# Kernel tuning notes

Hardware: AMD Instinct MI355X
Metric: run time of the kernel (lower is better)

## Reference

```python
import jax, jax.numpy as jnp
import numpy as np

N, IN_F, H, F = 4096, 256, 8, 64
NEG_INF = -1e9  # stand-in for -inf; avoids NaNs for fully-masked rows


def setup_inputs() -> dict:
    key = jax.random.key(0)
    k1, k2, k3, k4, k5 = jax.random.split(key, 5)
    h = jax.random.normal(k1, (N, IN_F), dtype=jnp.float32)
    adj = jax.random.randint(k2, (N, N), 0, 2, dtype=jnp.int32)
    # xavier-ish scaled params
    W = jax.random.normal(k3, (IN_F, H * F), dtype=jnp.float32) * (2.0 / (IN_F + H * F)) ** 0.5
    a_src = jax.random.normal(k4, (H, F), dtype=jnp.float32) * (2.0 / (H * F)) ** 0.5
    a_dst = jax.random.normal(k5, (H, F), dtype=jnp.float32) * (2.0 / (H * F)) ** 0.5
    bias = jnp.zeros((H * F,), dtype=jnp.float32)
    return {"h": h, "adj": adj, "W": W, "a_src": a_src, "a_dst": a_dst, "bias": bias}


def reference(h, adj, W, a_src, a_dst, bias):
    # Wh: [N, H, F]
    Wh = (h @ W).reshape(N, H, F)
    e_src = jnp.einsum('nhf,hf->nh', Wh, a_src)  # [N, H]
    e_dst = jnp.einsum('nhf,hf->nh', Wh, a_dst)  # [N, H]
    e = e_src[:, None, :] + e_dst[None, :, :]    # [N, N, H]
    e = jnp.where(e > 0, e, 0.2 * e)             # LeakyReLU(0.2)
    e = jnp.where((adj != 0)[:, :, None], e, NEG_INF)
    alpha = jax.nn.softmax(e, axis=1)            # softmax over neighbors j
    # h_prime[i,h,f] = sum_j alpha[i,j,h] * Wh[j,h,f]
    h_prime = jnp.einsum('ijh,jhf->ihf', alpha, Wh)
    h_prime = h_prime.reshape(N, H * F)          # concat=True
    return h_prime + bias
```

## Files before the change

kernel.cpp:

```cpp
#include <hip/hip_runtime.h>
#include <stdint.h>

#define NN   4096
#define KIN  256
#define NH   8
#define FD   64
#define HFD  512
#define NC   2
#define BI   32
#define JT   64
#define NT   ((NN / NC) / JT)

typedef __attribute__((ext_vector_type(4))) float  floatx4;
typedef __attribute__((ext_vector_type(8))) short  short8;

__device__ __forceinline__ unsigned short f2bf_rne(float x) {
    uint32_t u = __float_as_uint(x);
    u += 0x7FFFu + ((u >> 16) & 1u);
    return (unsigned short)(u >> 16);
}

__device__ __forceinline__ uint32_t packtrunc(float lo, float hi) {
    return (__float_as_uint(hi) & 0xFFFF0000u) | (__float_as_uint(lo) >> 16);
}

__global__ __launch_bounds__(256) void k1_front(
        const float* __restrict__ hmat, const float* __restrict__ Wmat,
        const float* __restrict__ a_src, const float* __restrict__ a_dst,
        unsigned short* __restrict__ whbT,
        float* __restrict__ esrcT, float* __restrict__ edstT) {
    __shared__ float As[64][36];
    __shared__ float Bs[32][64];
    __shared__ float scrS[64][16];
    __shared__ float scrD[64][16];
    const int tid = threadIdx.x;
    const int n0  = blockIdx.x * 64;
    const int hd  = blockIdx.y;
    const int hf0 = hd * 64;
    const int r0  = (tid >> 4) * 4;
    const int c0  = (tid & 15) * 4;
    float acc[4][4] = {};
    for (int k0 = 0; k0 < KIN; k0 += 32) {
        #pragma unroll
        for (int u = 0; u < 2; ++u) {
            const int v = tid * 2 + u;
            const int r = v >> 3, kk = (v & 7) * 4;
            *reinterpret_cast<float4*>(&As[r][kk]) =
                *reinterpret_cast<const float4*>(&hmat[(size_t)(n0 + r) * KIN + k0 + kk]);
        }
        #pragma unroll
        for (int u = 0; u < 2; ++u) {
            const int v = tid * 2 + u;
            const int kk = v >> 4, cc = (v & 15) * 4;
            *reinterpret_cast<float4*>(&Bs[kk][cc]) =
                *reinterpret_cast<const float4*>(&Wmat[(size_t)(k0 + kk) * HFD + hf0 + cc]);
        }
        __syncthreads();
        #pragma unroll
        for (int k = 0; k < 32; ++k) {
            const float4 b = *reinterpret_cast<const float4*>(&Bs[k][c0]);
            float av[4];
            #pragma unroll
            for (int i = 0; i < 4; ++i) av[i] = As[r0 + i][k];
            #pragma unroll
            for (int i = 0; i < 4; ++i) {
                acc[i][0] += av[i] * b.x;
                acc[i][1] += av[i] * b.y;
                acc[i][2] += av[i] * b.z;
                acc[i][3] += av[i] * b.w;
            }
        }
        __syncthreads();
    }
    #pragma unroll
    for (int j = 0; j < 4; ++j) {
        const int f = c0 + j;
        ushort4 w4;
        w4.x = f2bf_rne(acc[0][j]); w4.y = f2bf_rne(acc[1][j]);
        w4.z = f2bf_rne(acc[2][j]); w4.w = f2bf_rne(acc[3][j]);
        *reinterpret_cast<ushort4*>(&whbT[(size_t)(hf0 + f) * NN + n0 + r0]) = w4;
    }
    float as4[4], ad4[4];
    #pragma unroll
    for (int j = 0; j < 4; ++j) { as4[j] = a_src[hf0 + c0 + j]; ad4[j] = a_dst[hf0 + c0 + j]; }
    #pragma unroll
    for (int i = 0; i < 4; ++i) {
        float ps = 0.f, pd = 0.f;
        #pragma unroll
        for (int j = 0; j < 4; ++j) { ps += acc[i][j] * as4[j]; pd += acc[i][j] * ad4[j]; }
        scrS[r0 + i][tid & 15] = ps;
        scrD[r0 + i][tid & 15] = pd;
    }
    __syncthreads();
    if (tid < 64) {
        float s = 0.f, d = 0.f;
        #pragma unroll
        for (int q = 0; q < 16; ++q) { s += scrS[tid][q]; d += scrD[tid][q]; }
        esrcT[hd * NN + n0 + tid] = s;
        edstT[hd * NN + n0 + tid] = d;
    }
}

__global__ __launch_bounds__(256) void k2_tables(
        const float* __restrict__ esrcT, const float* __restrict__ edstT,
        float* __restrict__ es1T, float* __restrict__ es2T,
        float* __restrict__ ed1T, float* __restrict__ ed2T) {
    __shared__ float red[256];
    const int hd = blockIdx.x, tid = threadIdx.x;
    float m = -1e30f;
    for (int n = tid; n < NN; n += 256) m = fmaxf(m, edstT[hd * NN + n]);
    red[tid] = m;
    __syncthreads();
    for (int s = 128; s > 0; s >>= 1) {
        if (tid < s) red[tid] = fmaxf(red[tid], red[tid + s]);
        __syncthreads();
    }
    const float maxd = red[0];
    for (int n = tid; n < NN; n += 256) {
        const float ed = edstT[hd * NN + n];
        ed1T[hd * NN + n] = __expf(ed);
        ed2T[hd * NN + n] = __expf(0.2f * ed);
        const float es = esrcT[hd * NN + n];
        const float t  = es + maxd;
        const float M  = fmaxf(t, 0.2f * t);
        es1T[hd * NN + n] = __expf(es - M);
        es2T[hd * NN + n] = __expf(0.2f * es - M);
    }
}

__global__ __launch_bounds__(512) void k3_attn(
        const int* __restrict__ adj, const unsigned short* __restrict__ whbT,
        const float* __restrict__ es1T, const float* __restrict__ es2T,
        const float* __restrict__ ed1T, const float* __restrict__ ed2T,
        float* __restrict__ numP, float* __restrict__ denP) {
    __shared__ uint32_t amask[BI][32];
    const int tid  = threadIdx.x;
    const int lane = tid & 63;
    const int wid  = tid >> 6;
    const int iblk = blockIdx.x & 127;
    const int jc   = blockIdx.x >> 7;
    const int i0   = iblk * BI;
    const int jbase = jc * (NN / NC);
    const int g  = lane >> 4;
    const int lr = lane & 15;

    float es1[2], es2[2];
    #pragma unroll
    for (int mi = 0; mi < 2; ++mi) {
        es1[mi] = es1T[wid * NN + i0 + mi * 16 + lr];
        es2[mi] = es2T[wid * NN + i0 + mi * 16 + lr];
    }

    floatx4 acc[2][4] = {};
    floatx4 accd[2] = {};

    short8 ones;
    {
        const short ov = (lr == 0) ? (short)0x3F80 : (short)0;
        #pragma unroll
        for (int e = 0; e < 8; ++e) ones[e] = ov;
    }

    for (int t = 0; t < NT; ++t) {
        const int j0 = jbase + t * JT;
        __syncthreads();
        {
            const int r = tid >> 4, q = tid & 15;
            const int4 a = *reinterpret_cast<const int4*>(&adj[(size_t)(i0 + r) * NN + j0 + q * 4]);
            const uint32_t m0 = (a.x ? 0xFFFFu : 0u) | (a.y ? 0xFFFF0000u : 0u);
            const uint32_t m1 = (a.z ? 0xFFFFu : 0u) | (a.w ? 0xFFFF0000u : 0u);
            const int w0 = q * 2;
            const int p0 = (w0 & 3) | ((((w0 >> 2) ^ (r & 7)) & 7) << 2);
            amask[r][p0]     = m0;
            amask[r][p0 + 1] = m1;
        }
        __syncthreads();

        short8 bfrag[2][4];
        #pragma unroll
        for (int ks = 0; ks < 2; ++ks)
            #pragma unroll
            for (int ni = 0; ni < 4; ++ni)
                bfrag[ks][ni] = *reinterpret_cast<const short8*>(
                    &whbT[(size_t)(wid * FD + ni * 16 + lr) * NN + j0 + ks * 32 + g * 8]);

        #pragma unroll
        for (int ks = 0; ks < 2; ++ks) {
            const int jo = wid * NN + j0 + ks * 32 + g * 8;
            const float4 e1a = *reinterpret_cast<const float4*>(&ed1T[jo]);
            const float4 e1b = *reinterpret_cast<const float4*>(&ed1T[jo + 4]);
            const float4 e2a = *reinterpret_cast<const float4*>(&ed2T[jo]);
            const float4 e2b = *reinterpret_cast<const float4*>(&ed2T[jo + 4]);
            #pragma unroll
            for (int mi = 0; mi < 2; ++mi) {
                const int rr = mi * 16 + lr;
                const int pb = (((ks * 4 + g) ^ (lr & 7)) & 7) * 4;
                const uint4 msk = *reinterpret_cast<const uint4*>(&amask[rr][pb]);
                union { uint32_t w[4]; short8 s8; } pu;
                pu.w[0] = packtrunc(fmaxf(es1[mi] * e1a.x, es2[mi] * e2a.x),
                                    fmaxf(es1[mi] * e1a.y, es2[mi] * e2a.y)) & msk.x;
                pu.w[1] = packtrunc(fmaxf(es1[mi] * e1a.z, es2[mi] * e2a.z),
                                    fmaxf(es1[mi] * e1a.w, es2[mi] * e2a.w)) & msk.y;
                pu.w[2] = packtrunc(fmaxf(es1[mi] * e1b.x, es2[mi] * e2b.x),
                                    fmaxf(es1[mi] * e1b.y, es2[mi] * e2b.y)) & msk.z;
                pu.w[3] = packtrunc(fmaxf(es1[mi] * e1b.z, es2[mi] * e2b.z),
                                    fmaxf(es1[mi] * e1b.w, es2[mi] * e2b.w)) & msk.w;
                #pragma unroll
                for (int ni = 0; ni < 4; ++ni)
                    acc[mi][ni] = __builtin_amdgcn_mfma_f32_16x16x32_bf16(
                        pu.s8, bfrag[ks][ni], acc[mi][ni], 0, 0, 0);
                accd[mi] = __builtin_amdgcn_mfma_f32_16x16x32_bf16(
                        pu.s8, ones, accd[mi], 0, 0, 0);
            }
        }
    }

    #pragma unroll
    for (int mi = 0; mi < 2; ++mi) {
        #pragma unroll
        for (int ni = 0; ni < 4; ++ni) {
            #pragma unroll
            for (int r = 0; r < 4; ++r) {
                const int i = i0 + mi * 16 + g * 4 + r;
                numP[((size_t)jc * NN + i) * HFD + wid * FD + ni * 16 + lr] = acc[mi][ni][r];
            }
        }
        if (lr == 0) {
            #pragma unroll
            for (int r = 0; r < 4; ++r) {
                const int i = i0 + mi * 16 + g * 4 + r;
                denP[((size_t)jc * NH + wid) * NN + i] = accd[mi][r];
            }
        }
    }
}

__global__ __launch_bounds__(256) void k4_reduce(
        const float* __restrict__ numP, const float* __restrict__ denP,
        const float* __restrict__ bias, float* __restrict__ out) {
    const int idx = blockIdx.x * 256 + threadIdx.x;
    const int e0 = idx * 4;
    const int i  = e0 >> 9;
    const int hf = e0 & 511;
    const int hd = hf >> 6;
    float4 s = make_float4(0.f, 0.f, 0.f, 0.f);
    float d = 0.f;
    #pragma unroll
    for (int c = 0; c < NC; ++c) {
        const float4 v = *reinterpret_cast<const float4*>(&numP[((size_t)c * NN + i) * HFD + hf]);
        s.x += v.x; s.y += v.y; s.z += v.z; s.w += v.w;
        d += denP[((size_t)c * NH + hd) * NN + i];
    }
    const float inv = 1.0f / d;
    const float4 b = *reinterpret_cast<const float4*>(&bias[hf]);
    float4 o;
    o.x = s.x * inv + b.x; o.y = s.y * inv + b.y;
    o.z = s.z * inv + b.z; o.w = s.w * inv + b.w;
    *reinterpret_cast<float4*>(&out[(size_t)i * HFD + hf]) = o;
}

extern "C" void kernel_launch(void* const* d_in, const int* in_sizes, int n_in,
                              void* d_out, int out_size, void* d_ws, size_t ws_size,
                              hipStream_t stream) {
    const float* hmat  = (const float*)d_in[0];
    const int*   adj   = (const int*)d_in[1];
    const float* Wmat  = (const float*)d_in[2];
    const float* a_src = (const float*)d_in[3];
    const float* a_dst = (const float*)d_in[4];
    const float* bias  = (const float*)d_in[5];
    float* out = (float*)d_out;

    char* ws = (char*)d_ws;
    unsigned short* whbT = (unsigned short*)ws;
    float* esrcT = (float*)(ws + (4u << 20));
    float* edstT = esrcT + NH * NN;
    float* es1T  = edstT + NH * NN;
    float* es2T  = es1T + NH * NN;
    float* ed1T  = es2T + NH * NN;
    float* ed2T  = ed1T + NH * NN;
    float* numP  = ed2T + NH * NN;
    float* denP  = numP + (size_t)NC * NN * HFD;

    k1_front<<<dim3(64, 8), 256, 0, stream>>>(hmat, Wmat, a_src, a_dst, whbT, esrcT, edstT);
    k2_tables<<<dim3(NH), 256, 0, stream>>>(esrcT, edstT, es1T, es2T, ed1T, ed2T);
    k3_attn<<<dim3(128 * NC), 512, 0, stream>>>(adj, whbT, es1T, es2T, ed1T, ed2T, numP, denP);
    k4_reduce<<<dim3((NN * HFD / 4) / 256), 256, 0, stream>>>(numP, denP, bias, out);
}
```

Baseline: 233.7 us.

## Use split-bf16 MFMA projection, smaller attention tiles, double-buffered mask, atomic reduction

```diff
diff --git a/kernel.cpp b/kernel.cpp
--- a/kernel.cpp
+++ b/kernel.cpp
@@ -6,8 +6,8 @@
 #define NH   8
 #define FD   64
 #define HFD  512
-#define NC   2
-#define BI   32
+#define NC   4
+#define BI   16
 #define JT   64
 #define NT   ((NN / NC) / JT)
 
@@ -19,85 +19,107 @@
     u += 0x7FFFu + ((u >> 16) & 1u);
     return (unsigned short)(u >> 16);
 }
-
+__device__ __forceinline__ float bf2f(unsigned short b) {
+    return __uint_as_float(((uint32_t)b) << 16);
+}
 __device__ __forceinline__ uint32_t packtrunc(float lo, float hi) {
     return (__float_as_uint(hi) & 0xFFFF0000u) | (__float_as_uint(lo) >> 16);
 }
 
+__global__ __launch_bounds__(256) void k_zero(float* __restrict__ outAcc,
+                                              float* __restrict__ denA) {
+    const int idx = blockIdx.x * 256 + threadIdx.x;
+    const float4 z = make_float4(0.f, 0.f, 0.f, 0.f);
+    if (idx < (NN * HFD) / 4) {
+        *reinterpret_cast<float4*>(&outAcc[idx * 4]) = z;
+    } else {
+        const int q = idx - (NN * HFD) / 4;
+        if (q < (NH * NN) / 4) *reinterpret_cast<float4*>(&denA[q * 4]) = z;
+    }
+}
+
+__global__ __launch_bounds__(256) void k0_prep(
+        const float* __restrict__ hmat, const float* __restrict__ Wmat,
+        unsigned short* __restrict__ h_hi, unsigned short* __restrict__ h_lo,
+        unsigned short* __restrict__ wt_hi, unsigned short* __restrict__ wt_lo) {
+    const int bx = blockIdx.x, tid = threadIdx.x;
+    if (bx < 1024) {
+        const int e0 = (bx * 256 + tid) * 4;
+        const float4 v = *reinterpret_cast<const float4*>(&hmat[e0]);
+        ushort4 hi, lo;
+        hi.x = f2bf_rne(v.x); lo.x = f2bf_rne(v.x - bf2f(hi.x));
+        hi.y = f2bf_rne(v.y); lo.y = f2bf_rne(v.y - bf2f(hi.y));
+        hi.z = f2bf_rne(v.z); lo.z = f2bf_rne(v.z - bf2f(hi.z));
+        hi.w = f2bf_rne(v.w); lo.w = f2bf_rne(v.w - bf2f(hi.w));
+        *reinterpret_cast<ushort4*>(&h_hi[e0]) = hi;
+        *reinterpret_cast<ushort4*>(&h_lo[e0]) = lo;
+    } else {
+        const int c = bx - 1024;
+        const float v = Wmat[(size_t)tid * HFD + c];
+        const unsigned short hi = f2bf_rne(v);
+        const unsigned short lo = f2bf_rne(v - bf2f(hi));
+        wt_hi[c * KIN + tid] = hi;
+        wt_lo[c * KIN + tid] = lo;
+    }
+}
+
 __global__ __launch_bounds__(256) void k1_front(
-        const float* __restrict__ hmat, const float* __restrict__ Wmat,
+        const unsigned short* __restrict__ h_hi, const unsigned short* __restrict__ h_lo,
+        const unsigned short* __restrict__ wt_hi, const unsigned short* __restrict__ wt_lo,
         const float* __restrict__ a_src, const float* __restrict__ a_dst,
         unsigned short* __restrict__ whbT,
         float* __restrict__ esrcT, float* __restrict__ edstT) {
-    __shared__ float As[64][36];
-    __shared__ float Bs[32][64];
-    __shared__ float scrS[64][16];
-    __shared__ float scrD[64][16];
-    const int tid = threadIdx.x;
+    const int tid  = threadIdx.x;
+    const int w    = tid >> 6;
+    const int lane = tid & 63;
+    const int g = lane >> 4, lr = lane & 15;
     const int n0  = blockIdx.x * 64;
     const int hd  = blockIdx.y;
-    const int hf0 = hd * 64;
-    const int r0  = (tid >> 4) * 4;
-    const int c0  = (tid & 15) * 4;
-    float acc[4][4] = {};
+    const int hf0 = hd * FD;
+    const int row = n0 + w * 16 + lr;
+    floatx4 acc[4] = {};
+    #pragma unroll
     for (int k0 = 0; k0 < KIN; k0 += 32) {
-        #pragma unroll
-        for (int u = 0; u < 2; ++u) {
-            const int v = tid * 2 + u;
-            const int r = v >> 3, kk = (v & 7) * 4;
-            *reinterpret_cast<float4*>(&As[r][kk]) =
-                *reinterpret_cast<const float4*>(&hmat[(size_t)(n0 + r) * KIN + k0 + kk]);
-        }
-        #pragma unroll
-        for (int u = 0; u < 2; ++u) {
-            const int v = tid * 2 + u;
-            const int kk = v >> 4, cc = (v & 15) * 4;
-            *reinterpret_cast<float4*>(&Bs[kk][cc]) =
-                *reinterpret_cast<const float4*>(&Wmat[(size_t)(k0 + kk) * HFD + hf0 + cc]);
-        }
-        __syncthreads();
-        #pragma unroll
-        for (int k = 0; k < 32; ++k) {
-            const float4 b = *reinterpret_cast<const float4*>(&Bs[k][c0]);
-            float av[4];
-            #pragma unroll
-            for (int i = 0; i < 4; ++i) av[i] = As[r0 + i][k];
-            #pragma unroll
-            for (int i = 0; i < 4; ++i) {
-                acc[i][0] += av[i] * b.x;
-                acc[i][1] += av[i] * b.y;
-                acc[i][2] += av[i] * b.z;
-                acc[i][3] += av[i] * b.w;
-            }
-        }
-        __syncthreads();
-    }
-    #pragma unroll
-    for (int j = 0; j < 4; ++j) {
-        const int f = c0 + j;
-        ushort4 w4;
-        w4.x = f2bf_rne(acc[0][j]); w4.y = f2bf_rne(acc[1][j]);
-        w4.z = f2bf_rne(acc[2][j]); w4.w = f2bf_rne(acc[3][j]);
-        *reinterpret_cast<ushort4*>(&whbT[(size_t)(hf0 + f) * NN + n0 + r0]) = w4;
-    }
-    float as4[4], ad4[4];
-    #pragma unroll
-    for (int j = 0; j < 4; ++j) { as4[j] = a_src[hf0 + c0 + j]; ad4[j] = a_dst[hf0 + c0 + j]; }
-    #pragma unroll
-    for (int i = 0; i < 4; ++i) {
+        const short8 ahi = *reinterpret_cast<const short8*>(&h_hi[(size_t)row * KIN + k0 + g * 8]);
+        const short8 alo = *reinterpret_cast<const short8*>(&h_lo[(size_t)row * KIN + k0 + g * 8]);
+        #pragma unroll
+        for (int ni = 0; ni < 4; ++ni) {
+            const size_t bo = (size_t)(hf0 + ni * 16 + lr) * KIN + k0 + g * 8;
+            const short8 bhi = *reinterpret_cast<const short8*>(&wt_hi[bo]);
+            const short8 blo = *reinterpret_cast<const short8*>(&wt_lo[bo]);
+            acc[ni] = __builtin_amdgcn_mfma_f32_16x16x32_bf16(ahi, bhi, acc[ni], 0, 0, 0);
+            acc[ni] = __builtin_amdgcn_mfma_f32_16x16x32_bf16(ahi, blo, acc[ni], 0, 0, 0);
+            acc[ni] = __builtin_amdgcn_mfma_f32_16x16x32_bf16(alo, bhi, acc[ni], 0, 0, 0);
+        }
+    }
+    #pragma unroll
+    for (int ni = 0; ni < 4; ++ni) {
+        const int hf = hf0 + ni * 16 + lr;
+        ushort4 o;
+        o.x = f2bf_rne(acc[ni][0]); o.y = f2bf_rne(acc[ni][1]);
+        o.z = f2bf_rne(acc[ni][2]); o.w = f2bf_rne(acc[ni][3]);
+        *reinterpret_cast<ushort4*>(&whbT[(size_t)hf * NN + n0 + w * 16 + g * 4]) = o;
+    }
+    float asv[4], adv[4];
+    #pragma unroll
+    for (int ni = 0; ni < 4; ++ni) {
+        asv[ni] = a_src[hf0 + ni * 16 + lr];
+        adv[ni] = a_dst[hf0 + ni * 16 + lr];
+    }
+    #pragma unroll
+    for (int r = 0; r < 4; ++r) {
         float ps = 0.f, pd = 0.f;
         #pragma unroll
-        for (int j = 0; j < 4; ++j) { ps += acc[i][j] * as4[j]; pd += acc[i][j] * ad4[j]; }
-        scrS[r0 + i][tid & 15] = ps;
-        scrD[r0 + i][tid & 15] = pd;
-    }
-    __syncthreads();
-    if (tid < 64) {
-        float s = 0.f, d = 0.f;
-        #pragma unroll
-        for (int q = 0; q < 16; ++q) { s += scrS[tid][q]; d += scrD[tid][q]; }
-        esrcT[hd * NN + n0 + tid] = s;
-        edstT[hd * NN + n0 + tid] = d;
+        for (int ni = 0; ni < 4; ++ni) { ps += acc[ni][r] * asv[ni]; pd += acc[ni][r] * adv[ni]; }
+        #pragma unroll
+        for (int off = 1; off < 16; off <<= 1) {
+            ps += __shfl_xor(ps, off, 64);
+            pd += __shfl_xor(pd, off, 64);
+        }
+        if (lr == 0) {
+            esrcT[hd * NN + n0 + w * 16 + g * 4 + r] = ps;
+            edstT[hd * NN + n0 + w * 16 + g * 4 + r] = pd;
+        }
     }
 }
 
@@ -128,32 +150,27 @@
     }
 }
 
-__global__ __launch_bounds__(512) void k3_attn(
+__global__ __launch_bounds__(512, 8) void k3_attn(
         const int* __restrict__ adj, const unsigned short* __restrict__ whbT,
         const float* __restrict__ es1T, const float* __restrict__ es2T,
         const float* __restrict__ ed1T, const float* __restrict__ ed2T,
-        float* __restrict__ numP, float* __restrict__ denP) {
-    __shared__ uint32_t amask[BI][32];
+        float* __restrict__ outAcc, float* __restrict__ denA) {
+    __shared__ uint32_t amask[2][BI][32];
     const int tid  = threadIdx.x;
     const int lane = tid & 63;
     const int wid  = tid >> 6;
-    const int iblk = blockIdx.x & 127;
-    const int jc   = blockIdx.x >> 7;
+    const int iblk = blockIdx.x & 255;
+    const int jc   = blockIdx.x >> 8;
     const int i0   = iblk * BI;
     const int jbase = jc * (NN / NC);
     const int g  = lane >> 4;
     const int lr = lane & 15;
 
-    float es1[2], es2[2];
-    #pragma unroll
-    for (int mi = 0; mi < 2; ++mi) {
-        es1[mi] = es1T[wid * NN + i0 + mi * 16 + lr];
-        es2[mi] = es2T[wid * NN + i0 + mi * 16 + lr];
-    }
-
-    floatx4 acc[2][4] = {};
-    floatx4 accd[2] = {};
-
+    const float es1 = es1T[wid * NN + i0 + lr];
+    const float es2 = es2T[wid * NN + i0 + lr];
+
+    floatx4 acc[4] = {};
+    floatx4 accd = {};
     short8 ones;
     {
         const short ov = (lr == 0) ? (short)0x3F80 : (short)0;
@@ -161,20 +178,22 @@
         for (int e = 0; e < 8; ++e) ones[e] = ov;
     }
 
+    const int sr = tid >> 5, sw = tid & 31;
+    const int spos = (sw & 3) | ((((sw >> 2) ^ (sr & 7)) & 7) << 2);
+    const int* aptr = &adj[(size_t)(i0 + sr) * NN + sw * 2];
+
+    int2 R = *reinterpret_cast<const int2*>(aptr + jbase);
+    amask[0][sr][spos] = (R.x ? 0xFFFFu : 0u) | (R.y ? 0xFFFF0000u : 0u);
+    R = *reinterpret_cast<const int2*>(aptr + jbase + JT);
+    __syncthreads();
+
     for (int t = 0; t < NT; ++t) {
-        const int j0 = jbase + t * JT;
-        __syncthreads();
-        {
-            const int r = tid >> 4, q = tid & 15;
-            const int4 a = *reinterpret_cast<const int4*>(&adj[(size_t)(i0 + r) * NN + j0 + q * 4]);
-            const uint32_t m0 = (a.x ? 0xFFFFu : 0u) | (a.y ? 0xFFFF0000u : 0u);
-            const uint32_t m1 = (a.z ? 0xFFFFu : 0u) | (a.w ? 0xFFFF0000u : 0u);
-            const int w0 = q * 2;
-            const int p0 = (w0 & 3) | ((((w0 >> 2) ^ (r & 7)) & 7) << 2);
-            amask[r][p0]     = m0;
-            amask[r][p0 + 1] = m1;
-        }
-        __syncthreads();
+        const int j0  = jbase + t * JT;
+        const int buf = t & 1;
+        if (t + 1 < NT)
+            amask[(t + 1) & 1][sr][spos] = (R.x ? 0xFFFFu : 0u) | (R.y ? 0xFFFF0000u : 0u);
+        if (t + 2 < NT)
+            R = *reinterpret_cast<const int2*>(aptr + jbase + (t + 2) * JT);
 
         short8 bfrag[2][4];
         #pragma unroll
@@ -191,72 +210,54 @@
             const float4 e1b = *reinterpret_cast<const float4*>(&ed1T[jo + 4]);
             const float4 e2a = *reinterpret_cast<const float4*>(&ed2T[jo]);
             const float4 e2b = *reinterpret_cast<const float4*>(&ed2T[jo + 4]);
+            const int pb = (((ks * 4 + g) ^ (lr & 7)) & 7) * 4;
+            const uint4 msk = *reinterpret_cast<const uint4*>(&amask[buf][lr][pb]);
+            union { uint32_t wd[4]; short8 s8; } pu;
+            pu.wd[0] = packtrunc(fmaxf(es1 * e1a.x, es2 * e2a.x),
+                                 fmaxf(es1 * e1a.y, es2 * e2a.y)) & msk.x;
+            pu.wd[1] = packtrunc(fmaxf(es1 * e1a.z, es2 * e2a.z),
+                                 fmaxf(es1 * e1a.w, es2 * e2a.w)) & msk.y;
+            pu.wd[2] = packtrunc(fmaxf(es1 * e1b.x, es2 * e2b.x),
+                                 fmaxf(es1 * e1b.y, es2 * e2b.y)) & msk.z;
+            pu.wd[3] = packtrunc(fmaxf(es1 * e1b.z, es2 * e2b.z),
+                                 fmaxf(es1 * e1b.w, es2 * e2b.w)) & msk.w;
             #pragma unroll
-            for (int mi = 0; mi < 2; ++mi) {
-                const int rr = mi * 16 + lr;
-                const int pb = (((ks * 4 + g) ^ (lr & 7)) & 7) * 4;
-                const uint4 msk = *reinterpret_cast<const uint4*>(&amask[rr][pb]);
-                union { uint32_t w[4]; short8 s8; } pu;
-                pu.w[0] = packtrunc(fmaxf(es1[mi] * e1a.x, es2[mi] * e2a.x),
-                                    fmaxf(es1[mi] * e1a.y, es2[mi] * e2a.y)) & msk.x;
-                pu.w[1] = packtrunc(fmaxf(es1[mi] * e1a.z, es2[mi] * e2a.z),
-                                    fmaxf(es1[mi] * e1a.w, es2[mi] * e2a.w)) & msk.y;
-                pu.w[2] = packtrunc(fmaxf(es1[mi] * e1b.x, es2[mi] * e2b.x),
-                                    fmaxf(es1[mi] * e1b.y, es2[mi] * e2b.y)) & msk.z;
-                pu.w[3] = packtrunc(fmaxf(es1[mi] * e1b.z, es2[mi] * e2b.z),
-                                    fmaxf(es1[mi] * e1b.w, es2[mi] * e2b.w)) & msk.w;
-                #pragma unroll
-                for (int ni = 0; ni < 4; ++ni)
-                    acc[mi][ni] = __builtin_amdgcn_mfma_f32_16x16x32_bf16(
-                        pu.s8, bfrag[ks][ni], acc[mi][ni], 0, 0, 0);
-                accd[mi] = __builtin_amdgcn_mfma_f32_16x16x32_bf16(
-                        pu.s8, ones, accd[mi], 0, 0, 0);
-            }
-        }
-    }
-
-    #pragma unroll
-    for (int mi = 0; mi < 2; ++mi) {
-        #pragma unroll
-        for (int ni = 0; ni < 4; ++ni) {
-            #pragma unroll
-            for (int r = 0; r < 4; ++r) {
-                const int i = i0 + mi * 16 + g * 4 + r;
-                numP[((size_t)jc * NN + i) * HFD + wid * FD + ni * 16 + lr] = acc[mi][ni][r];
-            }
-        }
-        if (lr == 0) {
-            #pragma unroll
-            for (int r = 0; r < 4; ++r) {
-                const int i = i0 + mi * 16 + g * 4 + r;
-                denP[((size_t)jc * NH + wid) * NN + i] = accd[mi][r];
-            }
-        }
-    }
-}
-
-__global__ __launch_bounds__(256) void k4_reduce(
-        const float* __restrict__ numP, const float* __restrict__ denP,
-        const float* __restrict__ bias, float* __restrict__ out) {
+            for (int ni = 0; ni < 4; ++ni)
+                acc[ni] = __builtin_amdgcn_mfma_f32_16x16x32_bf16(
+                    pu.s8, bfrag[ks][ni], acc[ni], 0, 0, 0);
+            accd = __builtin_amdgcn_mfma_f32_16x16x32_bf16(pu.s8, ones, accd, 0, 0, 0);
+        }
+        __syncthreads();
+    }
+
+    #pragma unroll
+    for (int ni = 0; ni < 4; ++ni)
+        #pragma unroll
+        for (int r = 0; r < 4; ++r)
+            atomicAdd(&outAcc[(size_t)(i0 + g * 4 + r) * HFD + wid * FD + ni * 16 + lr],
+                      acc[ni][r]);
+    if (lr == 0) {
+        #pragma unroll
+        for (int r = 0; r < 4; ++r)
+            atomicAdd(&denA[wid * NN + i0 + g * 4 + r], accd[r]);
+    }
+}
+
+__global__ __launch_bounds__(256) void k4_norm(
+        float* __restrict__ out, const float* __restrict__ denA,
+        const float* __restrict__ bias) {
     const int idx = blockIdx.x * 256 + threadIdx.x;
     const int e0 = idx * 4;
     const int i  = e0 >> 9;
     const int hf = e0 & 511;
     const int hd = hf >> 6;
-    float4 s = make_float4(0.f, 0.f, 0.f, 0.f);
-    float d = 0.f;
-    #pragma unroll
-    for (int c = 0; c < NC; ++c) {
-        const float4 v = *reinterpret_cast<const float4*>(&numP[((size_t)c * NN + i) * HFD + hf]);
-        s.x += v.x; s.y += v.y; s.z += v.z; s.w += v.w;
-        d += denP[((size_t)c * NH + hd) * NN + i];
-    }
-    const float inv = 1.0f / d;
+    const float4 s = *reinterpret_cast<const float4*>(&out[e0]);
+    const float inv = 1.0f / denA[hd * NN + i];
     const float4 b = *reinterpret_cast<const float4*>(&bias[hf]);
     float4 o;
     o.x = s.x * inv + b.x; o.y = s.y * inv + b.y;
     o.z = s.z * inv + b.z; o.w = s.w * inv + b.w;
-    *reinterpret_cast<float4*>(&out[(size_t)i * HFD + hf]) = o;
+    *reinterpret_cast<float4*>(&out[e0]) = o;
 }
 
 extern "C" void kernel_launch(void* const* d_in, const int* in_sizes, int n_in,
@@ -278,11 +279,17 @@
     float* es2T  = es1T + NH * NN;
     float* ed1T  = es2T + NH * NN;
     float* ed2T  = ed1T + NH * NN;
-    float* numP  = ed2T + NH * NN;
-    float* denP  = numP + (size_t)NC * NN * HFD;
-
-    k1_front<<<dim3(64, 8), 256, 0, stream>>>(hmat, Wmat, a_src, a_dst, whbT, esrcT, edstT);
+    unsigned short* h_hi = (unsigned short*)(ed2T + NH * NN);
+    unsigned short* h_lo = h_hi + (size_t)NN * KIN;
+    unsigned short* wt_hi = h_lo + (size_t)NN * KIN;
+    unsigned short* wt_lo = wt_hi + (size_t)KIN * HFD;
+    float* denA = (float*)(wt_lo + (size_t)KIN * HFD);
+
+    k_zero<<<dim3((NN * HFD / 4 + NH * NN / 4 + 255) / 256), 256, 0, stream>>>(out, denA);
+    k0_prep<<<dim3(1536), 256, 0, stream>>>(hmat, Wmat, h_hi, h_lo, wt_hi, wt_lo);
+    k1_front<<<dim3(64, 8), 256, 0, stream>>>(h_hi, h_lo, wt_hi, wt_lo, a_src, a_dst,
+                                              whbT, esrcT, edstT);
     k2_tables<<<dim3(NH), 256, 0, stream>>>(esrcT, edstT, es1T, es2T, ed1T, ed2T);
-    k3_attn<<<dim3(128 * NC), 512, 0, stream>>>(adj, whbT, es1T, es2T, ed1T, ed2T, numP, denP);
-    k4_reduce<<<dim3((NN * HFD / 4) / 256), 256, 0, stream>>>(numP, denP, bias, out);
-}
+    k3_attn<<<dim3(256 * NC), 512, 0, stream>>>(adj, whbT, es1T, es2T, ed1T, ed2T, out, denA);
+    k4_norm<<<dim3((NN * HFD / 4) / 256), 256, 0, stream>>>(out, denA, bias);
+}
```

New measurement: 346.9 us. +48.4%, slower.
